# Kernel tuning notes

Hardware: AMD Instinct MI355X
Metric: run time of the kernel (lower is better)

Reference implementation:

```python
import jax, jax.numpy as jnp
import numpy as np

C = 256          # in_channels
CQK = C // 8     # query/key channels


def setup_inputs() -> dict:
    key = jax.random.key(0)
    ks = jax.random.split(key, 10)
    B, H, W = 4, 64, 64
    x1 = jax.random.normal(ks[0], (B, C, H, W), dtype=jnp.float32)
    x2 = jax.random.normal(ks[1], (B, C, H, W), dtype=jnp.float32)
    s = 0.05
    Wq = jax.random.normal(ks[2], (CQK, C), dtype=jnp.float32) * s
    bq = jax.random.normal(ks[3], (CQK,), dtype=jnp.float32) * s
    Wk = jax.random.normal(ks[4], (CQK, C), dtype=jnp.float32) * s
    bk = jax.random.normal(ks[5], (CQK,), dtype=jnp.float32) * s
    Wv = jax.random.normal(ks[6], (C, C), dtype=jnp.float32) * s
    bv = jax.random.normal(ks[7], (C,), dtype=jnp.float32) * s
    Wc = jax.random.normal(ks[8], (C, 2 * C), dtype=jnp.float32) * s
    bc = jax.random.normal(ks[9], (C,), dtype=jnp.float32) * s
    return {"x1": x1, "x2": x2, "Wq": Wq, "bq": bq, "Wk": Wk, "bk": bk,
            "Wv": Wv, "bv": bv, "Wc": Wc, "bc": bc}


def _proj(x_flat, Wm, b):
    # 1x1 conv == channel GEMM: [B,C,N] -> [B,Cout,N]
    return jnp.einsum('oc,bcn->bon', Wm, x_flat) + b[None, :, None]


def reference(x1, x2, Wq, bq, Wk, bk, Wv, bv, Wc, bc):
    B, Cin, H, W = x1.shape
    N = H * W
    xf1 = x1.reshape(B, Cin, N)
    xf2 = x2.reshape(B, Cin, N)
    q1 = _proj(xf1, Wq, bq)   # [B,CQK,N]
    k1 = _proj(xf1, Wk, bk)
    v1 = _proj(xf1, Wv, bv)   # [B,C,N]
    q2 = _proj(xf2, Wq, bq)
    k2 = _proj(xf2, Wk, bk)
    v2 = _proj(xf2, Wv, bv)

    def branch(q, k, v_other):
        # attn[b,i,j] = softmax_j(q[:, :, i] . k[:, :, j])
        attn = jax.nn.softmax(jnp.einsum('bci,bcj->bij', q, k), axis=2)
        # attended[b,c,i] = sum_j v_other[b,c,j] * attn[b,i,j]
        return jnp.einsum('bcj,bij->bci', v_other, attn)

    att1 = branch(q1, k1, v2).reshape(B, Cin, H, W)
    att2 = branch(q2, k2, v1).reshape(B, Cin, H, W)

    def combine(a, b_att):
        cat = jnp.concatenate((a, b_att), axis=1).reshape(B, 2 * Cin, N)
        comb = (jnp.einsum('oc,bcn->bon', Wc, cat) + bc[None, :, None]).reshape(B, Cin, H, W)
        return jnp.abs(comb).sum(axis=1, keepdims=True)

    # NOTE: original code uses x1 in BOTH combines (faithful to source)
    out1 = combine(x1, att1)
    out2 = combine(x1, att2)
    return out1, out2
```

## Files before the change

kernel.cpp:

```cpp
#include <hip/hip_runtime.h>
#include <cstdint>

#define LOG2E 1.4426950408889634f

typedef __bf16 bf16x8 __attribute__((ext_vector_type(8)));
typedef float f32x4 __attribute__((ext_vector_type(4)));

#define MFMA16(a,b,c) __builtin_amdgcn_mfma_f32_16x16x32_bf16((a),(b),(c),0,0,0)
#define EXP2(x) __builtin_amdgcn_exp2f(x)

#define LDS_BARRIER() asm volatile("s_waitcnt lgkmcnt(0)\n\ts_barrier" ::: "memory")

constexpr size_t OFF_XT = 0;
constexpr size_t OFF_QT = 8388608;
constexpr size_t OFF_KT = 9437184;
constexpr size_t OFF_V  = 10485760;
constexpr size_t OFF_WQ = 18874368;
constexpr size_t OFF_WK = 18882560;
constexpr size_t OFF_WV = 18890752;
constexpr size_t OFF_WC = 18956288;

static __device__ __forceinline__ unsigned short f2b(float a) {
  return __builtin_bit_cast(unsigned short, (__bf16)a);
}
static __device__ __forceinline__ unsigned pk2(float a, float b) {
  return ((unsigned)f2b(b) << 16) | (unsigned)f2b(a);
}

__global__ __launch_bounds__(256) void prep_kernel(
    const float* __restrict__ x1, const float* __restrict__ x2,
    const float* __restrict__ Wq, const float* __restrict__ Wk,
    const float* __restrict__ Wv, const float* __restrict__ Wc,
    short* __restrict__ ws)
{
  __shared__ float tile[64][65];
  const int tid = threadIdx.x;
  const int blk = blockIdx.x;
  if (blk < 2048) {
    const int nt = blk & 63, ct = (blk >> 6) & 3, b = (blk >> 8) & 3, inp = blk >> 10;
    const float* x = (inp ? x2 : x1) + (size_t)(b * 256 + ct * 64) * 4096 + nt * 64;
#pragma unroll
    for (int p = 0; p < 4; ++p) {
      int r = p * 16 + (tid >> 4);
      float4 v = *(const float4*)(x + (size_t)r * 4096 + (tid & 15) * 4);
      tile[r][(tid & 15) * 4 + 0] = v.x;
      tile[r][(tid & 15) * 4 + 1] = v.y;
      tile[r][(tid & 15) * 4 + 2] = v.z;
      tile[r][(tid & 15) * 4 + 3] = v.w;
    }
    __syncthreads();
    const int n = tid >> 2, c0 = (tid & 3) * 16;
    unsigned u[8];
#pragma unroll
    for (int k = 0; k < 8; ++k)
      u[k] = pk2(tile[c0 + 2 * k][n], tile[c0 + 2 * k + 1][n]);
    short* dst = ws + OFF_XT + (size_t)((inp * 4 + b) * 4096 + nt * 64 + n) * 256 + ct * 64 + c0;
    uint4 s0; s0.x = u[0]; s0.y = u[1]; s0.z = u[2]; s0.w = u[3];
    uint4 s1; s1.x = u[4]; s1.y = u[5]; s1.z = u[6]; s1.w = u[7];
    *(uint4*)(dst) = s0;
    *(uint4*)(dst + 8) = s1;
  } else {
    int idx = (blk - 2048) * 4096 + tid * 16;
    const float* src; short* dst; int off;
    if (idx < 8192)        { src = Wq; dst = ws + OFF_WQ; off = idx; }
    else if (idx < 16384)  { src = Wk; dst = ws + OFF_WK; off = idx - 8192; }
    else if (idx < 81920)  { src = Wv; dst = ws + OFF_WV; off = idx - 16384; }
    else                   { src = Wc; dst = ws + OFF_WC; off = idx - 81920; }
#pragma unroll
    for (int j = 0; j < 16; ++j) dst[off + j] = (short)f2b(src[off + j]);
  }
}

static __device__ __forceinline__ void proj_qk_body(
    short* __restrict__ ws, const float* __restrict__ bq, const float* __restrict__ bk,
    int blk, int tid)
{
  const int lane = tid & 63, wid = tid >> 6;
  const int g = lane >> 4, l15 = lane & 15;
  const int nt = blk & 31, b = (blk >> 5) & 3, inp = blk >> 7;
  const int n0 = nt * 128 + wid * 32;

  const short* xp  = ws + OFF_XT + (size_t)(inp * 4 + b) * (4096 * 256) + (size_t)n0 * 256;
  const short* wqp = ws + OFF_WQ;
  const short* wkp = ws + OFF_WK;
  short* Qt = ws + OFF_QT + (size_t)(inp * 4 + b) * (4096 * 32);
  short* Kt = ws + OFF_KT + (size_t)(inp * 4 + b) * (4096 * 32);

  const f32x4 z4 = {0.f, 0.f, 0.f, 0.f};
  f32x4 aq[2][2], ak[2][2];
#pragma unroll
  for (int i = 0; i < 2; ++i)
#pragma unroll
    for (int j = 0; j < 2; ++j) { aq[i][j] = z4; ak[i][j] = z4; }

#pragma unroll
  for (int ks = 0; ks < 8; ++ks) {
    bf16x8 xa[2];
#pragma unroll
    for (int ns = 0; ns < 2; ++ns)
      xa[ns] = *(const bf16x8*)(xp + (size_t)(ns * 16 + l15) * 256 + ks * 32 + g * 8);
#pragma unroll
    for (int os = 0; os < 2; ++os) {
      bf16x8 wq8 = *(const bf16x8*)(wqp + (size_t)(os * 16 + l15) * 256 + ks * 32 + g * 8);
      bf16x8 wk8 = *(const bf16x8*)(wkp + (size_t)(os * 16 + l15) * 256 + ks * 32 + g * 8);
#pragma unroll
      for (int ns = 0; ns < 2; ++ns) {
        aq[ns][os] = MFMA16(xa[ns], wq8, aq[ns][os]);
        ak[ns][os] = MFMA16(xa[ns], wk8, ak[ns][os]);
      }
    }
  }
  float bqv[2], bkv[2];
#pragma unroll
  for (int os = 0; os < 2; ++os) { bqv[os] = bq[os * 16 + l15]; bkv[os] = bk[os * 16 + l15]; }
#pragma unroll
  for (int ns = 0; ns < 2; ++ns)
#pragma unroll
    for (int os = 0; os < 2; ++os)
#pragma unroll
      for (int r = 0; r < 4; ++r) {
        int n = n0 + ns * 16 + g * 4 + r;
        int o = os * 16 + l15;
        Qt[(size_t)n * 32 + o] = (short)f2b((aq[ns][os][r] + bqv[os]) * LOG2E);
        Kt[(size_t)n * 32 + o] = (short)f2b(ak[ns][os][r] + bkv[os]);
      }
}

static __device__ __forceinline__ void proj_v_body(
    short* __restrict__ ws, const float* __restrict__ bv, char* vl, int blk, int tid)
{
  const int lane = tid & 63, wid = tid >> 6;
  const int g = lane >> 4, l15 = lane & 15;
  const int nt = blk & 63, b = (blk >> 6) & 3, inp = blk >> 8;
  const int n0 = nt * 64;

  const short* xp  = ws + OFF_XT + (size_t)(inp * 4 + b) * (4096 * 256) + (size_t)n0 * 256;
  const short* wvp = ws + OFF_WV;
  short* Vp = ws + OFF_V + (size_t)(inp * 4 + b) * (256 * 4096);

  const f32x4 z4 = {0.f, 0.f, 0.f, 0.f};
  f32x4 acc[4][4];
#pragma unroll
  for (int i = 0; i < 4; ++i)
#pragma unroll
    for (int j = 0; j < 4; ++j) acc[i][j] = z4;

#pragma unroll
  for (int ks = 0; ks < 8; ++ks) {
    bf16x8 xa[4];
#pragma unroll
    for (int ns = 0; ns < 4; ++ns)
      xa[ns] = *(const bf16x8*)(xp + (size_t)(ns * 16 + l15) * 256 + ks * 32 + g * 8);
#pragma unroll
    for (int os = 0; os < 4; ++os) {
      bf16x8 wv8 = *(const bf16x8*)(wvp + (size_t)(wid * 64 + os * 16 + l15) * 256 + ks * 32 + g * 8);
#pragma unroll
      for (int ns = 0; ns < 4; ++ns)
        acc[os][ns] = MFMA16(wv8, xa[ns], acc[os][ns]);
    }
  }
  float bvv[4][4];
#pragma unroll
  for (int os = 0; os < 4; ++os)
#pragma unroll
    for (int r = 0; r < 4; ++r) bvv[os][r] = bv[wid * 64 + os * 16 + g * 4 + r];

  char* myl = vl + wid * 8192;
#pragma unroll
  for (int os = 0; os < 4; ++os)
#pragma unroll
    for (int ns = 0; ns < 4; ++ns)
#pragma unroll
      for (int r = 0; r < 4; ++r) {
        int o_loc = os * 16 + g * 4 + r;
        int n_loc = ns * 16 + l15;
        *(short*)(myl + o_loc * 128 + ((n_loc * 2) ^ ((o_loc & 7) << 4))) =
            (short)f2b(acc[os][ns][r] + bvv[os][r]);
      }
#pragma unroll
  for (int sc = 0; sc < 4; ++sc)
#pragma unroll
    for (int sj = 0; sj < 2; ++sj) {
      int c_loc = sc * 16 + l15;
      bf16x8 row = *(const bf16x8*)(myl + c_loc * 128 +
                                    (((unsigned)(sj * 64 + g * 16)) ^ ((c_loc & 7) << 4)));
      size_t c16 = (size_t)(wid * 4 + sc);
      size_t j32 = (size_t)(nt * 2 + sj);
      *(bf16x8*)(Vp + (c16 * 128 + j32) * 512 + lane * 8) = row;
    }
}

__global__ __launch_bounds__(256) void proj_kernel(
    short* __restrict__ ws, const float* __restrict__ bq,
    const float* __restrict__ bk, const float* __restrict__ bv)
{
  __shared__ __align__(16) char vl[32768];
  const int tid = threadIdx.x, blk = blockIdx.x;
  if (blk < 256) proj_qk_body(ws, bq, bk, blk, tid);
  else           proj_v_body(ws, bv, vl, blk - 256, tid);
}

__global__ __launch_bounds__(256, 2) void attn_kernel(
    short* __restrict__ ws, const float* __restrict__ bc, float* __restrict__ out)
{
  const int tid = threadIdx.x, lane = tid & 63, wid = tid >> 6;
  const int g = lane >> 4, l15 = lane & 15;
  const int bid = ((blockIdx.x & 7) << 6) | (blockIdx.x >> 3);
  const int itile = bid & 63, b = (bid >> 6) & 3, br = bid >> 8;
  const int i0 = itile * 64;

  __shared__ __align__(16) char sm[34048];
  float* l_l  = (float*)(sm + 32768);
  float* part = (float*)(sm + 33024);

  const short* Qb  = ws + OFF_QT + (size_t)(br * 4 + b) * (4096 * 32);
  const short* Kb  = ws + OFF_KT + (size_t)(br * 4 + b) * (4096 * 32);
  const short* Vb  = ws + OFF_V  + (size_t)((1 - br) * 4 + b) * (256 * 4096);
  const short* xb  = ws + OFF_XT + (size_t)b * (4096 * 256);
  const short* Wcb = ws + OFF_WC;

  const f32x4 z4 = {0.f, 0.f, 0.f, 0.f};
  const int irow = wid * 16 + l15;
  const unsigned sw = (unsigned)((irow & 7) << 4);

  bf16x8 qf = *(const bf16x8*)(Qb + (size_t)(i0 + wid * 16 + l15) * 32 + g * 8);

  f32x4 oc[4][4];
#pragma unroll
  for (int i = 0; i < 4; ++i)
#pragma unroll
    for (int j = 0; j < 4; ++j) oc[i][j] = z4;
  float l_run = 0.f;

  {
    bf16x8 kt[4];
#pragma unroll
    for (int jt = 0; jt < 4; ++jt)
      kt[jt] = *(const bf16x8*)(Kb + (size_t)(jt * 16 + l15) * 32 + g * 8);
    f32x4 s0[4];
#pragma unroll
    for (int jt = 0; jt < 4; ++jt) s0[jt] = MFMA16(kt[jt], qf, z4);
#pragma unroll
    for (int jt = 0; jt < 4; ++jt) {
#pragma unroll
      for (int r = 0; r < 4; ++r) {
        float p = EXP2(s0[jt][r]);
        s0[jt][r] = p;
        l_run += p;
      }
      unsigned long long u =
          ((unsigned long long)pk2(s0[jt][2], s0[jt][3]) << 32) | pk2(s0[jt][0], s0[jt][1]);
      *(unsigned long long*)(sm + irow * 128 + (((unsigned)(jt * 32 + g * 8)) ^ sw)) = u;
    }
  }

  bf16x8 kf[2][4], va[2][2][4];
#pragma unroll
  for (int jt = 0; jt < 4; ++jt)
    kf[0][jt] = *(const bf16x8*)(Kb + (size_t)(64 + jt * 16 + l15) * 32 + g * 8);
#pragma unroll
  for (int ks = 0; ks < 2; ++ks)
#pragma unroll
    for (int cs = 0; cs < 4; ++cs)
      va[0][ks][cs] = *(const bf16x8*)(Vb + ((size_t)(wid * 4 + cs) * 128 + ks) * 512 + lane * 8);

  LDS_BARRIER();

#define ATTN_BODY(TC, CUR, NXT, PBR, PBW, DO_S, PREFK, PREFV)                            \
  do {                                                                                   \
    f32x4 st[4];                                                                         \
    if (DO_S) {                                                                          \
      _Pragma("unroll")                                                                  \
      for (int jt = 0; jt < 4; ++jt) st[jt] = MFMA16(kf[CUR][jt], qf, z4);               \
    }                                                                                    \
    if (PREFK) {                                                                         \
      _Pragma("unroll")                                                                  \
      for (int jt = 0; jt < 4; ++jt)                                                     \
        kf[NXT][jt] = *(const bf16x8*)(Kb + (size_t)(((TC) + 2) * 64 + jt * 16 + l15) * 32 + g * 8); \
    }                                                                                    \
    if (PREFV) {                                                                         \
      _Pragma("unroll")                                                                  \
      for (int ks = 0; ks < 2; ++ks)                                                     \
        _Pragma("unroll")                                                                \
        for (int cs = 0; cs < 4; ++cs)                                                   \
          va[NXT][ks][cs] = *(const bf16x8*)(Vb + ((size_t)(wid * 4 + cs) * 128 +        \
                                                   (size_t)((TC) + 1) * 2 + ks) * 512 + lane * 8); \
    }                                                                                    \
    __builtin_amdgcn_s_setprio(1);                                                       \
    {                                                                                    \
      const char* Pl = sm + (PBR) * 8192;                                                \
      _Pragma("unroll")                                                                  \
      for (int ks = 0; ks < 2; ++ks)                                                     \
        _Pragma("unroll")                                                                \
        for (int it = 0; it < 4; ++it) {                                                 \
          int i = it * 16 + l15;                                                         \
          bf16x8 pb = *(const bf16x8*)(Pl + i * 128 +                                    \
                                       (((unsigned)(ks * 64 + g * 16)) ^ ((i & 7) << 4))); \
          _Pragma("unroll")                                                              \
          for (int cs = 0; cs < 4; ++cs)                                                 \
            oc[cs][it] = MFMA16(va[CUR][ks][cs], pb, oc[cs][it]);                        \
        }                                                                                \
    }                                                                                    \
    __builtin_amdgcn_s_setprio(0);                                                       \
    if (DO_S) {                                                                          \
      char* Pw = sm + (PBW) * 8192;                                                      \
      _Pragma("unroll")                                                                  \
      for (int jt = 0; jt < 4; ++jt) {                                                   \
        _Pragma("unroll")                                                                \
        for (int r = 0; r < 4; ++r) {                                                    \
          float p = EXP2(st[jt][r]);                                                     \
          st[jt][r] = p;                                                                 \
          l_run += p;                                                                    \
        }                                                                                \
        unsigned long long u =                                                           \
            ((unsigned long long)pk2(st[jt][2], st[jt][3]) << 32) | pk2(st[jt][0], st[jt][1]); \
        *(unsigned long long*)(Pw + irow * 128 + (((unsigned)(jt * 32 + g * 8)) ^ sw)) = u; \
      }                                                                                  \
    }                                                                                    \
    LDS_BARRIER();                                                                       \
  } while (0)

  for (int t = 0; t < 62; t += 2) {
    ATTN_BODY(t, 0, 1, 0, 1, 1, 1, 1);
    ATTN_BODY(t + 1, 1, 0, 1, 0, 1, 1, 1);
  }
  ATTN_BODY(62, 0, 1, 0, 1, 1, 0, 1);
  ATTN_BODY(63, 1, 0, 1, 0, 0, 0, 0);
#undef ATTN_BODY

  l_run += __shfl_xor(l_run, 16);
  l_run += __shfl_xor(l_run, 32);

  if (g == 0) l_l[irow] = l_run;
  __syncthreads();
  float rl[4];
#pragma unroll
  for (int it = 0; it < 4; ++it) rl[it] = 1.f / l_l[it * 16 + l15];

#pragma unroll
  for (int cs = 0; cs < 4; ++cs)
#pragma unroll
    for (int it = 0; it < 4; ++it) {
      f32x4 v = oc[cs][it];
      v *= rl[it];
      int i = it * 16 + l15;
      unsigned byte = (unsigned)(i * 512) +
                      (((unsigned)((wid * 64 + cs * 16 + g * 4) * 2)) ^ ((i & 7) << 4));
      unsigned long long u = ((unsigned long long)pk2(v[2], v[3]) << 32) | pk2(v[0], v[1]);
      *(unsigned long long*)(sm + byte) = u;
    }
  __syncthreads();

  f32x4 cc[4][4];
#pragma unroll
  for (int i = 0; i < 4; ++i)
#pragma unroll
    for (int j = 0; j < 4; ++j) cc[i][j] = z4;

#pragma unroll
  for (int ks = 0; ks < 16; ++ks) {
    bf16x8 bfr[4];
#pragma unroll
    for (int ns = 0; ns < 4; ++ns) {
      int n = ns * 16 + l15;
      if (ks < 8)
        bfr[ns] = *(const bf16x8*)(xb + (size_t)(i0 + n) * 256 + ks * 32 + g * 8);
      else
        bfr[ns] = *(const bf16x8*)(sm + n * 512 +
                                   (((unsigned)((ks - 8) * 64 + g * 16)) ^ ((n & 7) << 4)));
    }
#pragma unroll
    for (int os = 0; os < 4; ++os) {
      bf16x8 af = *(const bf16x8*)(Wcb + (size_t)(wid * 64 + os * 16 + l15) * 512 + ks * 32 + g * 8);
#pragma unroll
      for (int ns = 0; ns < 4; ++ns)
        cc[os][ns] = MFMA16(af, bfr[ns], cc[os][ns]);
    }
  }
  float bcv[4][4];
#pragma unroll
  for (int os = 0; os < 4; ++os)
#pragma unroll
    for (int r = 0; r < 4; ++r) bcv[os][r] = bc[wid * 64 + os * 16 + g * 4 + r];

#pragma unroll
  for (int ns = 0; ns < 4; ++ns) {
    float tsum = 0.f;
#pragma unroll
    for (int os = 0; os < 4; ++os)
#pragma unroll
      for (int r = 0; r < 4; ++r)
        tsum += fabsf(cc[os][ns][r] + bcv[os][r]);
    tsum += __shfl_xor(tsum, 16);
    tsum += __shfl_xor(tsum, 32);
    if (g == 0) part[wid * 64 + ns * 16 + l15] = tsum;
  }
  __syncthreads();
  if (tid < 64) {
    float s = part[tid] + part[64 + tid] + part[128 + tid] + part[192 + tid];
    out[(size_t)br * 16384 + b * 4096 + i0 + tid] = s;
  }
}

extern "C" void kernel_launch(void* const* d_in, const int* in_sizes, int n_in,
                              void* d_out, int out_size, void* d_ws, size_t ws_size,
                              hipStream_t stream) {
  const float* x1 = (const float*)d_in[0];
  const float* x2 = (const float*)d_in[1];
  const float* Wq = (const float*)d_in[2];
  const float* bq = (const float*)d_in[3];
  const float* Wk = (const float*)d_in[4];
  const float* bk = (const float*)d_in[5];
  const float* Wv = (const float*)d_in[6];
  const float* bv = (const float*)d_in[7];
  const float* Wc = (const float*)d_in[8];
  const float* bc = (const float*)d_in[9];
  short* ws = (short*)d_ws;
  float* out = (float*)d_out;

  prep_kernel<<<2100, 256, 0, stream>>>(x1, x2, Wq, Wk, Wv, Wc, ws);
  proj_kernel<<<768, 256, 0, stream>>>(ws, bq, bk, bv);
  attn_kernel<<<512, 256, 0, stream>>>(ws, bc, out);
}
```

Measured before the change: 135.8 us.

## Deepen attention software pipeline: prefetch P fragments from LDS into registers

Restructures the attention loop so the P tiles for the next step are loaded from LDS into registers one iteration ahead, and the score computation now runs two tiles ahead of the PV accumulation. The prologue computes two score tiles up front, K and V keep single register buffers, and the V prefetch is issued after the PV MFMAs. The goal is to take LDS read latency off the MFMA critical path, at the cost of more registers for the double-buffered P fragments, which may lower occupancy.

```diff
diff --git a/kernel.cpp b/kernel.cpp
--- a/kernel.cpp
+++ b/kernel.cpp
@@ -232,14 +232,16 @@
     for (int j = 0; j < 4; ++j) oc[i][j] = z4;
   float l_run = 0.f;
 
-  {
+#pragma unroll
+  for (int tt = 0; tt < 2; ++tt) {
     bf16x8 kt[4];
 #pragma unroll
     for (int jt = 0; jt < 4; ++jt)
-      kt[jt] = *(const bf16x8*)(Kb + (size_t)(jt * 16 + l15) * 32 + g * 8);
+      kt[jt] = *(const bf16x8*)(Kb + (size_t)(tt * 64 + jt * 16 + l15) * 32 + g * 8);
     f32x4 s0[4];
 #pragma unroll
     for (int jt = 0; jt < 4; ++jt) s0[jt] = MFMA16(kt[jt], qf, z4);
+    char* Pw = sm + tt * 8192;
 #pragma unroll
     for (int jt = 0; jt < 4; ++jt) {
 #pragma unroll
@@ -250,60 +252,74 @@
       }
       unsigned long long u =
           ((unsigned long long)pk2(s0[jt][2], s0[jt][3]) << 32) | pk2(s0[jt][0], s0[jt][1]);
-      *(unsigned long long*)(sm + irow * 128 + (((unsigned)(jt * 32 + g * 8)) ^ sw)) = u;
-    }
-  }
-
-  bf16x8 kf[2][4], va[2][2][4];
+      *(unsigned long long*)(Pw + irow * 128 + (((unsigned)(jt * 32 + g * 8)) ^ sw)) = u;
+    }
+  }
+
+  bf16x8 kf[4], va[2][4], pb[2][2][4];
 #pragma unroll
   for (int jt = 0; jt < 4; ++jt)
-    kf[0][jt] = *(const bf16x8*)(Kb + (size_t)(64 + jt * 16 + l15) * 32 + g * 8);
+    kf[jt] = *(const bf16x8*)(Kb + (size_t)(128 + jt * 16 + l15) * 32 + g * 8);
 #pragma unroll
   for (int ks = 0; ks < 2; ++ks)
 #pragma unroll
     for (int cs = 0; cs < 4; ++cs)
-      va[0][ks][cs] = *(const bf16x8*)(Vb + ((size_t)(wid * 4 + cs) * 128 + ks) * 512 + lane * 8);
+      va[ks][cs] = *(const bf16x8*)(Vb + ((size_t)(wid * 4 + cs) * 128 + ks) * 512 + lane * 8);
 
   LDS_BARRIER();
 
-#define ATTN_BODY(TC, CUR, NXT, PBR, PBW, DO_S, PREFK, PREFV)                            \
+#pragma unroll
+  for (int ks = 0; ks < 2; ++ks)
+#pragma unroll
+    for (int it = 0; it < 4; ++it) {
+      int i = it * 16 + l15;
+      pb[0][ks][it] = *(const bf16x8*)(sm + i * 128 +
+                                       (((unsigned)(ks * 64 + g * 16)) ^ ((i & 7) << 4)));
+    }
+  LDS_BARRIER();
+
+#define ATTN_BODY(TC, CUR, NXT, DO_S, PREFK, PREFV, DO_PB)                               \
   do {                                                                                   \
-    f32x4 st[4];                                                                         \
-    if (DO_S) {                                                                          \
-      _Pragma("unroll")                                                                  \
-      for (int jt = 0; jt < 4; ++jt) st[jt] = MFMA16(kf[CUR][jt], qf, z4);               \
-    }                                                                                    \
-    if (PREFK) {                                                                         \
-      _Pragma("unroll")                                                                  \
-      for (int jt = 0; jt < 4; ++jt)                                                     \
-        kf[NXT][jt] = *(const bf16x8*)(Kb + (size_t)(((TC) + 2) * 64 + jt * 16 + l15) * 32 + g * 8); \
-    }                                                                                    \
-    if (PREFV) {                                                                         \
-      _Pragma("unroll")                                                                  \
-      for (int ks = 0; ks < 2; ++ks)                                                     \
-        _Pragma("unroll")                                                                \
-        for (int cs = 0; cs < 4; ++cs)                                                   \
-          va[NXT][ks][cs] = *(const bf16x8*)(Vb + ((size_t)(wid * 4 + cs) * 128 +        \
-                                                   (size_t)((TC) + 1) * 2 + ks) * 512 + lane * 8); \
-    }                                                                                    \
-    __builtin_amdgcn_s_setprio(1);                                                       \
-    {                                                                                    \
-      const char* Pl = sm + (PBR) * 8192;                                                \
+    if (DO_PB) {                                                                         \
+      const char* Pr = sm + (((TC) + 1) & 1) * 8192;                                     \
       _Pragma("unroll")                                                                  \
       for (int ks = 0; ks < 2; ++ks)                                                     \
         _Pragma("unroll")                                                                \
         for (int it = 0; it < 4; ++it) {                                                 \
           int i = it * 16 + l15;                                                         \
-          bf16x8 pb = *(const bf16x8*)(Pl + i * 128 +                                    \
-                                       (((unsigned)(ks * 64 + g * 16)) ^ ((i & 7) << 4))); \
-          _Pragma("unroll")                                                              \
-          for (int cs = 0; cs < 4; ++cs)                                                 \
-            oc[cs][it] = MFMA16(va[CUR][ks][cs], pb, oc[cs][it]);                        \
+          pb[NXT][ks][it] = *(const bf16x8*)(Pr + i * 128 +                              \
+                                (((unsigned)(ks * 64 + g * 16)) ^ ((i & 7) << 4)));      \
         }                                                                                \
     }                                                                                    \
+    f32x4 st[4];                                                                         \
+    if (DO_S) {                                                                          \
+      _Pragma("unroll")                                                                  \
+      for (int jt = 0; jt < 4; ++jt) st[jt] = MFMA16(kf[jt], qf, z4);                    \
+    }                                                                                    \
+    if (PREFK) {                                                                         \
+      _Pragma("unroll")                                                                  \
+      for (int jt = 0; jt < 4; ++jt)                                                     \
+        kf[jt] = *(const bf16x8*)(Kb + (size_t)(((TC) + 3) * 64 + jt * 16 + l15) * 32 + g * 8); \
+    }                                                                                    \
+    __builtin_amdgcn_s_setprio(1);                                                       \
+    _Pragma("unroll")                                                                    \
+    for (int ks = 0; ks < 2; ++ks)                                                       \
+      _Pragma("unroll")                                                                  \
+      for (int it = 0; it < 4; ++it)                                                     \
+        _Pragma("unroll")                                                                \
+        for (int cs = 0; cs < 4; ++cs)                                                   \
+          oc[cs][it] = MFMA16(va[ks][cs], pb[CUR][ks][it], oc[cs][it]);                  \
     __builtin_amdgcn_s_setprio(0);                                                       \
+    if (PREFV) {                                                                         \
+      _Pragma("unroll")                                                                  \
+      for (int ks = 0; ks < 2; ++ks)                                                     \
+        _Pragma("unroll")                                                                \
+        for (int cs = 0; cs < 4; ++cs)                                                   \
+          va[ks][cs] = *(const bf16x8*)(Vb + ((size_t)(wid * 4 + cs) * 128 +             \
+                                              (size_t)((TC) + 1) * 2 + ks) * 512 + lane * 8); \
+    }                                                                                    \
     if (DO_S) {                                                                          \
-      char* Pw = sm + (PBW) * 8192;                                                      \
+      char* Pw = sm + ((TC) & 1) * 8192;                                                 \
       _Pragma("unroll")                                                                  \
       for (int jt = 0; jt < 4; ++jt) {                                                   \
         _Pragma("unroll")                                                                \
@@ -320,12 +336,14 @@
     LDS_BARRIER();                                                                       \
   } while (0)
 
-  for (int t = 0; t < 62; t += 2) {
-    ATTN_BODY(t, 0, 1, 0, 1, 1, 1, 1);
-    ATTN_BODY(t + 1, 1, 0, 1, 0, 1, 1, 1);
-  }
-  ATTN_BODY(62, 0, 1, 0, 1, 1, 0, 1);
-  ATTN_BODY(63, 1, 0, 1, 0, 0, 0, 0);
+  for (int t = 0; t < 60; t += 2) {
+    ATTN_BODY(t,     0, 1, 1, 1, 1, 1);
+    ATTN_BODY(t + 1, 1, 0, 1, 1, 1, 1);
+  }
+  ATTN_BODY(60, 0, 1, 1, 1, 1, 1);
+  ATTN_BODY(61, 1, 0, 1, 0, 1, 1);
+  ATTN_BODY(62, 0, 1, 0, 0, 1, 1);
+  ATTN_BODY(63, 1, 0, 0, 0, 0, 0);
 #undef ATTN_BODY
 
   l_run += __shfl_xor(l_run, 16);
```

Result: no change. 135.3 us (-0.4%).
